# Optimization experiments

Hardware: AMD Instinct MI355X
Metric: run time of the kernel (lower is better)

The kernel has to match this reference:

```python
import jax, jax.numpy as jnp
import numpy as np

T, D = 2048, 2048
H, H_KV, DH = 32, 8, 64
I = 5632
EPS = 1e-5


def setup_inputs() -> dict:
    key = jax.random.key(0)
    ks = jax.random.split(key, 9)
    s = 0.02
    return {
        "x": jax.random.normal(ks[0], (T, D), dtype=jnp.float32),
        "ln1_w": jnp.ones((D,), dtype=jnp.float32),
        "ln2_w": jnp.ones((D,), dtype=jnp.float32),
        "wq": jax.random.normal(ks[1], (D, H * DH), dtype=jnp.float32) * s,
        "wk": jax.random.normal(ks[2], (D, H_KV * DH), dtype=jnp.float32) * s,
        "wv": jax.random.normal(ks[3], (D, H_KV * DH), dtype=jnp.float32) * s,
        "wo": jax.random.normal(ks[4], (H * DH, D), dtype=jnp.float32) * s,
        "w1": jax.random.normal(ks[5], (D, 2 * I), dtype=jnp.float32) * s,
        "w2": jax.random.normal(ks[6], (I, D), dtype=jnp.float32) * s,
    }


def _rmsnorm(x, w):
    var = jnp.mean(x * x, axis=-1, keepdims=True)
    return x * jax.lax.rsqrt(var + EPS) * w


def reference(x, ln1_w, ln2_w, wq, wk, wv, wo, w1, w2):
    t, d = x.shape
    h = _rmsnorm(x, ln1_w)
    # projections -> (heads, T, head_dim)
    q = (h @ wq).reshape(t, H, DH).transpose(1, 0, 2)
    k = (h @ wk).reshape(t, H_KV, DH).transpose(1, 0, 2)
    v = (h @ wv).reshape(t, H_KV, DH).transpose(1, 0, 2)
    # GQA: query head hq uses kv head hq * H_KV // H == hq // (H // H_KV)
    rep = H // H_KV
    k = jnp.repeat(k, rep, axis=0)  # (H, T, DH)
    v = jnp.repeat(v, rep, axis=0)
    scale = 1.0 / np.sqrt(DH)
    scores = jnp.einsum('htd,hsd->hts', q, k) * scale  # (H, T, T)
    causal = jnp.tril(jnp.ones((t, t), dtype=bool))
    neg = jnp.asarray(jnp.finfo(scores.dtype).min, scores.dtype)
    scores = jnp.where(causal[None, :, :], scores, neg)
    weights = jax.nn.softmax(scores, axis=-1)
    attn = jnp.einsum('hts,hsd->htd', weights, v)  # (H, T, DH)
    attn = attn.transpose(1, 0, 2).reshape(t, H * DH)
    x = x + attn @ wo
    h2 = _rmsnorm(x, ln2_w)
    fc1 = h2 @ w1  # (T, 2I)
    gate, val = fc1[:, :I], fc1[:, I:]
    sw = jax.nn.silu(gate) * val
    return x + sw @ w2
```

## Files before the change

### kernel.cpp

```cpp
#include <hip/hip_runtime.h>
#include <hip/hip_bf16.h>
#include <cstdint>
#include <cstddef>

#define TT 2048
#define DD 2048
#define NHQ 32
#define NHKV 8
#define DHD 64
#define II 5632

typedef short short8 __attribute__((ext_vector_type(8)));
typedef __bf16 bf16x8 __attribute__((ext_vector_type(8)));
typedef float f32x4 __attribute__((ext_vector_type(4)));

__device__ __forceinline__ float b2f(unsigned short u) {
  union { float f; unsigned int i; } v; v.i = ((unsigned int)u) << 16; return v.f;
}
__device__ __forceinline__ unsigned short f2b(float f) {
  union { float f; unsigned int i; } v; v.f = f;
  unsigned int r = v.i + 0x7FFFu + ((v.i >> 16) & 1u);
  return (unsigned short)(r >> 16);
}

__device__ __forceinline__ void gload16(const unsigned short* g, unsigned short* l) {
  __builtin_amdgcn_global_load_lds(
      (const __attribute__((address_space(1))) void*)g,
      (__attribute__((address_space(3))) void*)(unsigned int)(uintptr_t)l,
      16, 0, 0);
}

#define WAITVM(N) asm volatile("s_waitcnt vmcnt(" #N ")" ::: "memory")
#define BARRIER() do { asm volatile("" ::: "memory"); __builtin_amdgcn_s_barrier(); \
                       asm volatile("" ::: "memory"); } while (0)

__global__ void transpose_f32_bf16(const float* __restrict__ src,
                                   unsigned short* __restrict__ dst,
                                   int K, int N) {
  __shared__ unsigned short tile[64][70];
  const int bn = blockIdx.x * 64;
  const int bk = blockIdx.y * 64;
  const int tid = threadIdx.x;
  const int rr = tid >> 4, c4 = (tid & 15) * 4;
#pragma unroll
  for (int j = 0; j < 4; ++j) {
    const int r = rr + j * 16;
    float4 v = *(const float4*)(src + (size_t)(bk + r) * N + bn + c4);
    ushort4 u;
    u.x = f2b(v.x); u.y = f2b(v.y); u.z = f2b(v.z); u.w = f2b(v.w);
    *(ushort4*)&tile[r][c4] = u;
  }
  __syncthreads();
#pragma unroll
  for (int j = 0; j < 4; ++j) {
    const int n = rr + j * 16;
    ushort4 u;
    u.x = tile[c4 + 0][n];
    u.y = tile[c4 + 1][n];
    u.z = tile[c4 + 2][n];
    u.w = tile[c4 + 3][n];
    *(ushort4*)(dst + (size_t)(bn + n) * K + bk + c4) = u;
  }
}

__global__ void rmsnorm_kernel(const float* __restrict__ x,
                               const float* __restrict__ w,
                               unsigned short* __restrict__ out) {
  const int row = blockIdx.x;
  const float* xr = x + (size_t)row * DD;
  const int t = threadIdx.x;
  float4 v0 = ((const float4*)xr)[t];
  float4 v1 = ((const float4*)xr)[t + 256];
  float ss = v0.x * v0.x + v0.y * v0.y + v0.z * v0.z + v0.w * v0.w +
             v1.x * v1.x + v1.y * v1.y + v1.z * v1.z + v1.w * v1.w;
#pragma unroll
  for (int off = 32; off >= 1; off >>= 1) ss += __shfl_xor(ss, off);
  __shared__ float sred[4];
  if ((t & 63) == 0) sred[t >> 6] = ss;
  __syncthreads();
  float tot = sred[0] + sred[1] + sred[2] + sred[3];
  float rs = rsqrtf(tot * (1.0f / DD) + 1e-5f);
  float4 w0 = ((const float4*)w)[t];
  float4 w1v = ((const float4*)w)[t + 256];
  unsigned short* orow = out + (size_t)row * DD;
  ushort4 o0, o1;
  o0.x = f2b(v0.x * rs * w0.x); o0.y = f2b(v0.y * rs * w0.y);
  o0.z = f2b(v0.z * rs * w0.z); o0.w = f2b(v0.w * rs * w0.w);
  o1.x = f2b(v1.x * rs * w1v.x); o1.y = f2b(v1.y * rs * w1v.y);
  o1.z = f2b(v1.z * rs * w1v.z); o1.w = f2b(v1.w * rs * w1v.w);
  ((ushort4*)orow)[t] = o0;
  ((ushort4*)orow)[t + 256] = o1;
}

template <int EPI>
__global__ void gemm_bt(const unsigned short* __restrict__ A, int lda,
                        const unsigned short* __restrict__ Bt, int ldb,
                        int K,
                        const float* __restrict__ resid,
                        void* __restrict__ Cout, int ldc) {
  __shared__ __align__(16) unsigned short As[128 * 32];
  __shared__ __align__(16) unsigned short Bs[128 * 32];
  const int bm = blockIdx.y * 128;
  const int bn = blockIdx.x * 128;
  const int tid = threadIdx.x;
  const int lane = tid & 63;
  const int L = lane & 15, G = lane >> 4;
  const int w = tid >> 6;
  const int wr = (w >> 1) * 64, wc = (w & 1) * 64;

  const f32x4 zero = {0.f, 0.f, 0.f, 0.f};
  f32x4 acc[4][4];
#pragma unroll
  for (int m = 0; m < 4; ++m)
#pragma unroll
    for (int n = 0; n < 4; ++n) acc[m][n] = zero;

  const int srow = w * 32 + (lane >> 2);
  const int scol = (lane & 3) * 8;
  const unsigned short* gA = A + (size_t)(bm + srow) * lda + scol;
  const unsigned short* gB = Bt + (size_t)(bn + srow) * ldb + scol;
  unsigned short* lA0 = &As[w * 1024];
  unsigned short* lA1 = &As[w * 1024 + 512];
  unsigned short* lB0 = &Bs[w * 1024];
  unsigned short* lB1 = &Bs[w * 1024 + 512];

  const int nk = K >> 5;
  for (int kt = 0; kt < nk; ++kt) {
    const int ko = kt * 32;
    __syncthreads();
    gload16(gA + ko, lA0);
    gload16(gA + (size_t)16 * lda + ko, lA1);
    gload16(gB + ko, lB0);
    gload16(gB + (size_t)16 * ldb + ko, lB1);
    __syncthreads();
    bf16x8 af[4], bfr[4];
#pragma unroll
    for (int m = 0; m < 4; ++m)
      af[m] = *reinterpret_cast<const bf16x8*>(&As[(wr + m * 16 + L) * 32 + G * 8]);
#pragma unroll
    for (int n = 0; n < 4; ++n)
      bfr[n] = *reinterpret_cast<const bf16x8*>(&Bs[(wc + n * 16 + L) * 32 + G * 8]);
#pragma unroll
    for (int m = 0; m < 4; ++m)
#pragma unroll
      for (int n = 0; n < 4; ++n)
        acc[m][n] = __builtin_amdgcn_mfma_f32_16x16x32_bf16(af[m], bfr[n], acc[m][n], 0, 0, 0);
  }

#pragma unroll
  for (int m = 0; m < 4; ++m)
#pragma unroll
    for (int n = 0; n < 4; ++n)
#pragma unroll
      for (int i = 0; i < 4; ++i) {
        const int r = bm + wr + m * 16 + G * 4 + i;
        const int c = bn + wc + n * 16 + L;
        const float val = acc[m][n][i];
        if constexpr (EPI == 0) {
          ((unsigned short*)Cout)[(size_t)r * ldc + c] = f2b(val);
        } else {
          ((float*)Cout)[(size_t)r * ldc + c] = val + resid[(size_t)r * ldc + c];
        }
      }
}

template <int EPI>
__launch_bounds__(512, 2)
__global__ void gemm_bt_wide(const unsigned short* __restrict__ A, int lda,
                             const unsigned short* __restrict__ Bt, int ldb,
                             int K,
                             const float* __restrict__ resid,
                             void* __restrict__ Cout, int ldc) {
  __shared__ __align__(16) unsigned short As[4][128 * 32];
  __shared__ __align__(16) unsigned short Bs[4][256 * 32];
  const int bm = blockIdx.y * 128;
  const int bn = blockIdx.x * 256;
  const int tid = threadIdx.x;
  const int lane = tid & 63;
  const int L = lane & 15, G = lane >> 4;
  const int w = tid >> 6;
  const int wr = (w >> 2) * 64;
  const int wc = (w & 3) * 64;

  const f32x4 zero = {0.f, 0.f, 0.f, 0.f};
  f32x4 acc[4][4];
#pragma unroll
  for (int m = 0; m < 4; ++m)
#pragma unroll
    for (int n = 0; n < 4; ++n) acc[m][n] = zero;

  const int arow = tid >> 2;
  const int slot = (tid & 3) * 8;
  const unsigned short* gA = A + (size_t)(bm + arow) * lda + slot;
  const unsigned short* gB0 = Bt + (size_t)(bn + arow) * ldb + slot;
  const unsigned short* gB1 = Bt + (size_t)(bn + 128 + arow) * ldb + slot;
  const int ldsA = w * 512;
  const int ldsB0 = w * 512;
  const int ldsB1 = 4096 + w * 512;

  const int nk = K >> 5;

  gload16(gA, &As[0][ldsA]);
  gload16(gB0, &Bs[0][ldsB0]);
  gload16(gB1, &Bs[0][ldsB1]);
  gload16(gA + 32, &As[1][ldsA]);
  gload16(gB0 + 32, &Bs[1][ldsB0]);
  gload16(gB1 + 32, &Bs[1][ldsB1]);

  int cb = 0;
  int ko = 64;

  auto COMPUTE = [&](int b) {
    bf16x8 af[4], bfr[4];
#pragma unroll
    for (int m = 0; m < 4; ++m)
      af[m] = *reinterpret_cast<const bf16x8*>(&As[b][(wr + m * 16 + L) * 32 + G * 8]);
#pragma unroll
    for (int n = 0; n < 4; ++n)
      bfr[n] = *reinterpret_cast<const bf16x8*>(&Bs[b][(wc + n * 16 + L) * 32 + G * 8]);
    __builtin_amdgcn_s_setprio(1);
#pragma unroll
    for (int m = 0; m < 4; ++m)
#pragma unroll
      for (int n = 0; n < 4; ++n)
        acc[m][n] = __builtin_amdgcn_mfma_f32_16x16x32_bf16(af[m], bfr[n], acc[m][n], 0, 0, 0);
    __builtin_amdgcn_s_setprio(0);
  };

  for (int t = 0; t < nk - 2; ++t) {
    const int sb = (cb + 2) & 3;
    gload16(gA + ko, &As[sb][ldsA]);
    gload16(gB0 + ko, &Bs[sb][ldsB0]);
    gload16(gB1 + ko, &Bs[sb][ldsB1]);
    ko += 32;
    WAITVM(6);
    BARRIER();
    COMPUTE(cb);
    cb = (cb + 1) & 3;
  }
  WAITVM(3);
  BARRIER();
  COMPUTE(cb);
  cb = (cb + 1) & 3;
  WAITVM(0);
  BARRIER();
  COMPUTE(cb);

#pragma unroll
  for (int m = 0; m < 4; ++m)
#pragma unroll
    for (int n = 0; n < 4; ++n)
#pragma unroll
      for (int i = 0; i < 4; ++i) {
        const int r = bm + wr + m * 16 + G * 4 + i;
        const int c = bn + wc + n * 16 + L;
        const float val = acc[m][n][i];
        if constexpr (EPI == 0) {
          ((unsigned short*)Cout)[(size_t)r * ldc + c] = f2b(val);
        } else {
          ((float*)Cout)[(size_t)r * ldc + c] = val + resid[(size_t)r * ldc + c];
        }
      }
}

__launch_bounds__(256, 2)
__global__ void attn_kernel(const unsigned short* __restrict__ qkv,
                            unsigned short* __restrict__ out) {
  const int hq = blockIdx.x;
  const int qb = blockIdx.y;
  const int hkv = hq >> 2;
  const int tid = threadIdx.x, lane = tid & 63, w = tid >> 6;
  const int L = lane & 15, G = lane >> 4;

  __shared__ __align__(16) unsigned short Ks[64 * 72];
  __shared__ __align__(16) unsigned short Vt[64 * 72];
  __shared__ __align__(16) unsigned short Ps[4][16 * 72];

  const int qrow = qb * 64 + w * 16;
  bf16x8 qf[2];
#pragma unroll
  for (int d0 = 0; d0 < 2; ++d0)
    qf[d0] = *reinterpret_cast<const bf16x8*>(
        qkv + (size_t)(qrow + L) * 3072 + hq * 64 + d0 * 32 + G * 8);

  const f32x4 zero = {0.f, 0.f, 0.f, 0.f};
  f32x4 o[4];
#pragma unroll
  for (int n = 0; n < 4; ++n) o[n] = zero;
  float mrow[4], lrow[4];
#pragma unroll
  for (int i = 0; i < 4; ++i) { mrow[i] = -1e30f; lrow[i] = 0.f; }

  const int ntile = qb + 1;
  for (int t = 0; t < ntile; ++t) {
    const int s0 = t * 64;
    __syncthreads();
#pragma unroll
    for (int i2 = 0; i2 < 2; ++i2) {
      const int c = i2 * 256 + tid;
      const int r = c >> 3, col = (c & 7) * 8;
      bf16x8 k8 = *reinterpret_cast<const bf16x8*>(
          qkv + (size_t)(s0 + r) * 3072 + 2048 + hkv * 64 + col);
      *reinterpret_cast<bf16x8*>(&Ks[r * 72 + col]) = k8;
      short8 v8 = *reinterpret_cast<const short8*>(
          qkv + (size_t)(s0 + r) * 3072 + 2560 + hkv * 64 + col);
#pragma unroll
      for (int j = 0; j < 8; ++j) {
        const int d = col + j;
        Vt[d * 72 + (r ^ (((d >> 3) & 7) << 3))] = (unsigned short)v8[j];
      }
    }
    __syncthreads();

    f32x4 sacc[4];
#pragma unroll
    for (int nt = 0; nt < 4; ++nt) {
      sacc[nt] = zero;
#pragma unroll
      for (int d0 = 0; d0 < 2; ++d0) {
        bf16x8 kf = *reinterpret_cast<const bf16x8*>(
            &Ks[(nt * 16 + L) * 72 + d0 * 32 + G * 8]);
        sacc[nt] = __builtin_amdgcn_mfma_f32_16x16x32_bf16(qf[d0], kf, sacc[nt], 0, 0, 0);
      }
    }

    const bool diag = (t == qb);
    float pt[4][4];
#pragma unroll
    for (int i = 0; i < 4; ++i) {
      const int q = qrow + G * 4 + i;
      float mx = mrow[i];
#pragma unroll
      for (int nt = 0; nt < 4; ++nt) {
        float sv = sacc[nt][i] * 0.125f;
        if (diag) {
          const int s = s0 + nt * 16 + L;
          sv = (s <= q) ? sv : -1e30f;
        }
        pt[i][nt] = sv;
        mx = fmaxf(mx, sv);
      }
#pragma unroll
      for (int off = 1; off < 16; off <<= 1) mx = fmaxf(mx, __shfl_xor(mx, off));
      const float scale_o = __expf(mrow[i] - mx);
      float rsum = 0.f;
#pragma unroll
      for (int nt = 0; nt < 4; ++nt) {
        const float p = __expf(pt[i][nt] - mx);
        pt[i][nt] = p;
        rsum += p;
      }
#pragma unroll
      for (int off = 1; off < 16; off <<= 1) rsum += __shfl_xor(rsum, off);
      mrow[i] = mx;
      lrow[i] = lrow[i] * scale_o + rsum;
#pragma unroll
      for (int nt = 0; nt < 4; ++nt) o[nt][i] *= scale_o;
    }

#pragma unroll
    for (int i = 0; i < 4; ++i) {
      const int prow = G * 4 + i;
#pragma unroll
      for (int nt = 0; nt < 4; ++nt)
        Ps[w][prow * 72 + ((nt * 16 + L) ^ ((prow & 7) << 3))] = f2b(pt[i][nt]);
    }
#pragma unroll
    for (int kc = 0; kc < 2; ++kc) {
      bf16x8 pf = *reinterpret_cast<const bf16x8*>(
          &Ps[w][L * 72 + ((kc * 32 + G * 8) ^ ((L & 7) << 3))]);
#pragma unroll
      for (int nt = 0; nt < 4; ++nt) {
        const int vrow = nt * 16 + L;
        bf16x8 vf = *reinterpret_cast<const bf16x8*>(
            &Vt[vrow * 72 + ((kc * 32 + G * 8) ^ (((vrow >> 3) & 7) << 3))]);
        o[nt] = __builtin_amdgcn_mfma_f32_16x16x32_bf16(pf, vf, o[nt], 0, 0, 0);
      }
    }
  }

#pragma unroll
  for (int nt = 0; nt < 4; ++nt)
#pragma unroll
    for (int i = 0; i < 4; ++i) {
      const float val = o[nt][i] / lrow[i];
      out[(size_t)(qrow + G * 4 + i) * 2048 + hq * 64 + nt * 16 + L] = f2b(val);
    }
}

__global__ void swiglu_kernel(unsigned short* __restrict__ fc1) {
  const size_t total = (size_t)TT * (II / 8);
  const size_t idx = (size_t)blockIdx.x * blockDim.x + threadIdx.x;
  if (idx >= total) return;
  const int m = (int)(idx / (II / 8));
  const int jc = (int)(idx % (II / 8));
  unsigned short* g = fc1 + (size_t)m * (2 * II) + jc * 8;
  short8 gv = *(const short8*)g;
  short8 vv = *(const short8*)(g + II);
  short8 ov;
#pragma unroll
  for (int j = 0; j < 8; ++j) {
    const float gf = b2f((unsigned short)gv[j]);
    const float vf = b2f((unsigned short)vv[j]);
    const float s = gf / (1.f + __expf(-gf));
    ov[j] = (short)f2b(s * vf);
  }
  *(short8*)g = ov;
}

extern "C" void kernel_launch(void* const* d_in, const int* in_sizes, int n_in,
                              void* d_out, int out_size, void* d_ws, size_t ws_size,
                              hipStream_t stream) {
  const float* x    = (const float*)d_in[0];
  const float* ln1w = (const float*)d_in[1];
  const float* ln2w = (const float*)d_in[2];
  const float* wq   = (const float*)d_in[3];
  const float* wk   = (const float*)d_in[4];
  const float* wv   = (const float*)d_in[5];
  const float* wo   = (const float*)d_in[6];
  const float* w1   = (const float*)d_in[7];
  const float* w2   = (const float*)d_in[8];
  float* outp = (float*)d_out;

  char* ws = (char*)d_ws;
  size_t off = 0;
  auto alloc = [&](size_t bytes) {
    char* p = ws + off;
    off += (bytes + 255) & ~(size_t)255;
    return p;
  };
  unsigned short* wqkvT = (unsigned short*)alloc((size_t)3072 * 2048 * 2);
  unsigned short* woT   = (unsigned short*)alloc((size_t)2048 * 2048 * 2);
  unsigned short* w1T   = (unsigned short*)alloc((size_t)11264 * 2048 * 2);
  unsigned short* w2T   = (unsigned short*)alloc((size_t)2048 * 5632 * 2);
  unsigned short* h     = (unsigned short*)alloc((size_t)2048 * 2048 * 2);
  unsigned short* qkv   = (unsigned short*)alloc((size_t)2048 * 3072 * 2);
  unsigned short* attnb = (unsigned short*)alloc((size_t)2048 * 2048 * 2);
  float*          x2    = (float*)alloc((size_t)2048 * 2048 * 4);
  unsigned short* h2    = (unsigned short*)alloc((size_t)2048 * 2048 * 2);
  unsigned short* fc1   = (unsigned short*)alloc((size_t)2048 * 11264 * 2);
  (void)ws_size; (void)in_sizes; (void)n_in; (void)out_size;

  transpose_f32_bf16<<<dim3(2048 / 64, 2048 / 64), 256, 0, stream>>>(wq, wqkvT, 2048, 2048);
  transpose_f32_bf16<<<dim3(512 / 64, 2048 / 64), 256, 0, stream>>>(wk, wqkvT + (size_t)2048 * 2048, 2048, 512);
  transpose_f32_bf16<<<dim3(512 / 64, 2048 / 64), 256, 0, stream>>>(wv, wqkvT + (size_t)2560 * 2048, 2048, 512);
  transpose_f32_bf16<<<dim3(2048 / 64, 2048 / 64), 256, 0, stream>>>(wo, woT, 2048, 2048);
  transpose_f32_bf16<<<dim3(11264 / 64, 2048 / 64), 256, 0, stream>>>(w1, w1T, 2048, 11264);
  transpose_f32_bf16<<<dim3(2048 / 64, 5632 / 64), 256, 0, stream>>>(w2, w2T, 5632, 2048);

  rmsnorm_kernel<<<2048, 256, 0, stream>>>(x, ln1w, h);

  gemm_bt<0><<<dim3(3072 / 128, 2048 / 128), 256, 0, stream>>>(
      h, 2048, wqkvT, 2048, 2048, nullptr, qkv, 3072);

  attn_kernel<<<dim3(NHQ, TT / 64), 256, 0, stream>>>(qkv, attnb);

  gemm_bt<1><<<dim3(2048 / 128, 2048 / 128), 256, 0, stream>>>(
      attnb, 2048, woT, 2048, 2048, x, x2, 2048);

  rmsnorm_kernel<<<2048, 256, 0, stream>>>(x2, ln2w, h2);

  gemm_bt_wide<0><<<dim3(11264 / 256, 2048 / 128), 512, 0, stream>>>(
      h2, 2048, w1T, 2048, 2048, nullptr, fc1, 11264);

  swiglu_kernel<<<5632, 256, 0, stream>>>(fc1);

  gemm_bt<1><<<dim3(2048 / 128, 2048 / 128), 256, 0, stream>>>(
      fc1, 11264, w2T, 5632, 5632, x2, outp, 2048);
}
```

Baseline: 670.0 us.

## Split-K the output-projection and down-projection GEMMs, fuse reduction with RMSNorm

```diff
diff --git a/kernel.cpp b/kernel.cpp
--- a/kernel.cpp
+++ b/kernel.cpp
@@ -92,16 +92,77 @@
   ((ushort4*)orow)[t + 256] = o1;
 }
 
+__global__ void reduce_rmsnorm_kernel(const float* __restrict__ p0,
+                                      const float* __restrict__ p1,
+                                      const float* __restrict__ x,
+                                      const float* __restrict__ w,
+                                      float* __restrict__ x2,
+                                      unsigned short* __restrict__ h2) {
+  const int row = blockIdx.x;
+  const size_t base = (size_t)row * DD;
+  const int t = threadIdx.x;
+  float4 a0 = ((const float4*)(p0 + base))[t];
+  float4 a1 = ((const float4*)(p0 + base))[t + 256];
+  float4 b0 = ((const float4*)(p1 + base))[t];
+  float4 b1 = ((const float4*)(p1 + base))[t + 256];
+  float4 c0 = ((const float4*)(x + base))[t];
+  float4 c1 = ((const float4*)(x + base))[t + 256];
+  float4 s0, s1;
+  s0.x = a0.x + b0.x + c0.x; s0.y = a0.y + b0.y + c0.y;
+  s0.z = a0.z + b0.z + c0.z; s0.w = a0.w + b0.w + c0.w;
+  s1.x = a1.x + b1.x + c1.x; s1.y = a1.y + b1.y + c1.y;
+  s1.z = a1.z + b1.z + c1.z; s1.w = a1.w + b1.w + c1.w;
+  ((float4*)(x2 + base))[t] = s0;
+  ((float4*)(x2 + base))[t + 256] = s1;
+  float ss = s0.x * s0.x + s0.y * s0.y + s0.z * s0.z + s0.w * s0.w +
+             s1.x * s1.x + s1.y * s1.y + s1.z * s1.z + s1.w * s1.w;
+#pragma unroll
+  for (int off = 32; off >= 1; off >>= 1) ss += __shfl_xor(ss, off);
+  __shared__ float sred[4];
+  if ((t & 63) == 0) sred[t >> 6] = ss;
+  __syncthreads();
+  float tot = sred[0] + sred[1] + sred[2] + sred[3];
+  float rs = rsqrtf(tot * (1.0f / DD) + 1e-5f);
+  float4 w0 = ((const float4*)w)[t];
+  float4 w1v = ((const float4*)w)[t + 256];
+  ushort4 o0, o1;
+  o0.x = f2b(s0.x * rs * w0.x); o0.y = f2b(s0.y * rs * w0.y);
+  o0.z = f2b(s0.z * rs * w0.z); o0.w = f2b(s0.w * rs * w0.w);
+  o1.x = f2b(s1.x * rs * w1v.x); o1.y = f2b(s1.y * rs * w1v.y);
+  o1.z = f2b(s1.z * rs * w1v.z); o1.w = f2b(s1.w * rs * w1v.w);
+  unsigned short* orow = h2 + base;
+  ((ushort4*)orow)[t] = o0;
+  ((ushort4*)orow)[t + 256] = o1;
+}
+
+__global__ void add3_kernel(const float4* __restrict__ p0,
+                            const float4* __restrict__ p1,
+                            const float4* __restrict__ x2,
+                            float4* __restrict__ out, int n4) {
+  const int i = blockIdx.x * 256 + threadIdx.x;
+  if (i >= n4) return;
+  float4 a = p0[i], b = p1[i], c = x2[i], r;
+  r.x = a.x + b.x + c.x; r.y = a.y + b.y + c.y;
+  r.z = a.z + b.z + c.z; r.w = a.w + b.w + c.w;
+  out[i] = r;
+}
+
 template <int EPI>
 __global__ void gemm_bt(const unsigned short* __restrict__ A, int lda,
                         const unsigned short* __restrict__ Bt, int ldb,
                         int K,
                         const float* __restrict__ resid,
-                        void* __restrict__ Cout, int ldc) {
+                        void* __restrict__ Cout, int ldc, size_t pstride) {
   __shared__ __align__(16) unsigned short As[128 * 32];
   __shared__ __align__(16) unsigned short Bs[128 * 32];
   const int bm = blockIdx.y * 128;
   const int bn = blockIdx.x * 128;
+  if (EPI == 2) {
+    const size_t kz = (size_t)blockIdx.z * K;
+    A += kz;
+    Bt += kz;
+  }
+  float* Pout = (float*)Cout + (EPI == 2 ? (size_t)blockIdx.z * pstride : 0);
   const int tid = threadIdx.x;
   const int lane = tid & 63;
   const int L = lane & 15, G = lane >> 4;
@@ -158,8 +219,10 @@
         const float val = acc[m][n][i];
         if constexpr (EPI == 0) {
           ((unsigned short*)Cout)[(size_t)r * ldc + c] = f2b(val);
+        } else if constexpr (EPI == 1) {
+          ((float*)Cout)[(size_t)r * ldc + c] = val + resid[(size_t)r * ldc + c];
         } else {
-          ((float*)Cout)[(size_t)r * ldc + c] = val + resid[(size_t)r * ldc + c];
+          Pout[(size_t)r * ldc + c] = val;
         }
       }
 }
@@ -267,7 +330,9 @@
 __global__ void attn_kernel(const unsigned short* __restrict__ qkv,
                             unsigned short* __restrict__ out) {
   const int hq = blockIdx.x;
-  const int qb = blockIdx.y;
+  const int yy = blockIdx.y;
+  const int q8 = yy & 7, seg = yy >> 3;
+  const int qb = (seg == 0) ? q8 : (seg == 1) ? 31 - q8 : (seg == 2) ? 8 + q8 : 23 - q8;
   const int hkv = hq >> 2;
   const int tid = threadIdx.x, lane = tid & 63, w = tid >> 6;
   const int L = lane & 15, G = lane >> 4;
@@ -439,7 +504,9 @@
   float*          x2    = (float*)alloc((size_t)2048 * 2048 * 4);
   unsigned short* h2    = (unsigned short*)alloc((size_t)2048 * 2048 * 2);
   unsigned short* fc1   = (unsigned short*)alloc((size_t)2048 * 11264 * 2);
-  (void)ws_size; (void)in_sizes; (void)n_in; (void)out_size;
+  float*          part  = (float*)alloc((size_t)2 * 2048 * 2048 * 4);
+  const bool use_split = (off <= ws_size);
+  (void)in_sizes; (void)n_in; (void)out_size;
 
   transpose_f32_bf16<<<dim3(2048 / 64, 2048 / 64), 256, 0, stream>>>(wq, wqkvT, 2048, 2048);
   transpose_f32_bf16<<<dim3(512 / 64, 2048 / 64), 256, 0, stream>>>(wk, wqkvT + (size_t)2048 * 2048, 2048, 512);
@@ -451,20 +518,34 @@
   rmsnorm_kernel<<<2048, 256, 0, stream>>>(x, ln1w, h);
 
   gemm_bt<0><<<dim3(3072 / 128, 2048 / 128), 256, 0, stream>>>(
-      h, 2048, wqkvT, 2048, 2048, nullptr, qkv, 3072);
+      h, 2048, wqkvT, 2048, 2048, nullptr, qkv, 3072, 0);
 
   attn_kernel<<<dim3(NHQ, TT / 64), 256, 0, stream>>>(qkv, attnb);
 
-  gemm_bt<1><<<dim3(2048 / 128, 2048 / 128), 256, 0, stream>>>(
-      attnb, 2048, woT, 2048, 2048, x, x2, 2048);
-
-  rmsnorm_kernel<<<2048, 256, 0, stream>>>(x2, ln2w, h2);
+  const size_t PS = (size_t)2048 * 2048;
+  if (use_split) {
+    gemm_bt<2><<<dim3(16, 16, 2), 256, 0, stream>>>(
+        attnb, 2048, woT, 2048, 1024, nullptr, part, 2048, PS);
+    reduce_rmsnorm_kernel<<<2048, 256, 0, stream>>>(part, part + PS, x, ln2w, x2, h2);
+  } else {
+    gemm_bt<1><<<dim3(16, 16), 256, 0, stream>>>(
+        attnb, 2048, woT, 2048, 2048, x, x2, 2048, 0);
+    rmsnorm_kernel<<<2048, 256, 0, stream>>>(x2, ln2w, h2);
+  }
 
   gemm_bt_wide<0><<<dim3(11264 / 256, 2048 / 128), 512, 0, stream>>>(
       h2, 2048, w1T, 2048, 2048, nullptr, fc1, 11264);
 
   swiglu_kernel<<<5632, 256, 0, stream>>>(fc1);
 
-  gemm_bt<1><<<dim3(2048 / 128, 2048 / 128), 256, 0, stream>>>(
-      fc1, 11264, w2T, 5632, 5632, x2, outp, 2048);
-}
+  if (use_split) {
+    gemm_bt<2><<<dim3(16, 16, 2), 256, 0, stream>>>(
+        fc1, 11264, w2T, 5632, 2816, nullptr, part, 2048, PS);
+    add3_kernel<<<(2048 * 2048 / 4 + 255) / 256, 256, 0, stream>>>(
+        (const float4*)part, (const float4*)(part + PS), (const float4*)x2,
+        (float4*)outp, 2048 * 2048 / 4);
+  } else {
+    gemm_bt<1><<<dim3(16, 16), 256, 0, stream>>>(
+        fc1, 11264, w2T, 5632, 5632, x2, outp, 2048, 0);
+  }
+}
```

Result: faster. 614.3 us (-8.3%).
